# Performance work log

Hardware: AMD Instinct MI355X
Metric: run time of the kernel (lower is better)

The kernel has to match this reference:

```python
import jax, jax.numpy as jnp
import numpy as np

ALPHA = 1.0
EPS = 1e-12  # tf.nn.l2_normalize epsilon
N, IN_DIM, UNITS = 8192, 1, 64


def setup_inputs() -> dict:
    key = jax.random.key(0)
    k1, k2 = jax.random.split(key)
    inputs = jax.random.normal(k1, (N, IN_DIM), dtype=jnp.float32)
    W = jax.random.normal(k2, (IN_DIM, UNITS), dtype=jnp.float32) * (1.0 / np.sqrt(IN_DIM))
    b = jnp.zeros((UNITS,), dtype=jnp.float32)
    return {"inputs": inputs, "W": W, "b": b}


def reference(inputs, W, b):
    # Dense projection (activation='linear')
    emb = inputs @ W + b  # [N, D]
    # Pairwise cosine similarity, computed as normalized matmul instead of
    # materializing the original [N, N, D] broadcast tensors.
    norm = jnp.sqrt(jnp.maximum(jnp.sum(emb * emb, axis=-1, keepdims=True), EPS))
    xn = emb / norm  # [N, D]
    cos = xn @ xn.T  # [N, N] cosine similarity
    # tf pairwise_sim = -cos; loss = 1 - |pairwise_sim| = 1 - |cos|
    loss = 1.0 - jnp.abs(cos)
    loss = jnp.max(loss, axis=-1)  # [N]
    loss = jnp.mean(loss)
    aux_loss = ALPHA * (-loss)  # layer returns -loss, scaled by alpha via add_loss
    return emb, aux_loss
```

## Files before the change

kernel.cpp:

```cpp
#include <hip/hip_runtime.h>
#include <math.h>
#include <float.h>

#define NROWS 8192
#define D     64
#define EPSN  1e-12f
#define TI    8
#define NBLK  (NROWS / TI)
#define JPT   (NROWS / 256)

__device__ __forceinline__ float wave_reduce_sum(float v) {
    #pragma unroll
    for (int m = 1; m < 64; m <<= 1) v += __shfl_xor(v, m, 64);
    return v;
}

__global__ __launch_bounds__(256) void k_main(
        const float* __restrict__ x, const float* __restrict__ W,
        const float* __restrict__ b, float* __restrict__ emb,
        float* __restrict__ partial) {
    __shared__ float red[TI][257];
    __shared__ float red2[TI][17];
    __shared__ float l8[TI];
    const int tid = threadIdx.x;
    const int blk = blockIdx.x;
    const int i0  = blk * TI;
    const int ln  = tid & 63;

    if (tid < TI * 16) {
        const int r  = tid >> 4;
        const int c4 = tid & 15;
        const float xr = x[i0 + r];
        const float4 w4 = ((const float4*)W)[c4];
        const float4 b4 = ((const float4*)b)[c4];
        float4 e;
        e.x = fmaf(xr, w4.x, b4.x);
        e.y = fmaf(xr, w4.y, b4.y);
        e.z = fmaf(xr, w4.z, b4.z);
        e.w = fmaf(xr, w4.w, b4.w);
        ((float4*)emb)[i0 * 16 + tid] = e;
    }

    const float wv = W[ln], bv = b[ln];
    const float wTw = wave_reduce_sum(wv * wv);
    const float wTb = wave_reduce_sum(wv * bv);
    const float bTb = wave_reduce_sum(bv * bv);

    const float xi_l = x[i0 + (ln & 7)];
    const float Af  = fmaf(xi_l, wTw, wTb);
    const float Cf  = fmaf(xi_l, wTb, bTb);
    const float cf  = Cf / Af;
    const float aAf = fabsf(Af);

    float p[JPT], q[JPT];
    #pragma unroll
    for (int k4 = 0; k4 < JPT / 4; ++k4) {
        const float4 v4 = ((const float4*)x)[tid + k4 * 256];
        const float vs[4] = {v4.x, v4.y, v4.z, v4.w};
        #pragma unroll
        for (int e = 0; e < 4; ++e) {
            const float v   = vs[e];
            const float nsq = fmaf(v, fmaf(v, wTw, 2.0f * wTb), bTb);
            const float iv  = rsqrtf(fmaxf(nsq, EPSN));
            q[k4 * 4 + e] = iv;
            p[k4 * 4 + e] = v * iv;
        }
    }

    #pragma unroll
    for (int ii = 0; ii < TI; ++ii) {
        const float absA = __shfl(aAf, ii, 64);
        const float c    = __shfl(cf,  ii, 64);
        const float C    = __shfl(Cf,  ii, 64);
        float mm;
        if (absA > 1e-12f) {
            float m0 = FLT_MAX, m1 = FLT_MAX, m2 = FLT_MAX, m3 = FLT_MAX;
            #pragma unroll
            for (int k = 0; k < JPT; k += 8) {
                const float t0 = fmaf(c, q[k    ], p[k    ]);
                const float t1 = fmaf(c, q[k + 1], p[k + 1]);
                const float t2 = fmaf(c, q[k + 2], p[k + 2]);
                const float t3 = fmaf(c, q[k + 3], p[k + 3]);
                const float t4 = fmaf(c, q[k + 4], p[k + 4]);
                const float t5 = fmaf(c, q[k + 5], p[k + 5]);
                const float t6 = fmaf(c, q[k + 6], p[k + 6]);
                const float t7 = fmaf(c, q[k + 7], p[k + 7]);
                m0 = fminf(m0, fminf(fabsf(t0), fabsf(t1)));
                m1 = fminf(m1, fminf(fabsf(t2), fabsf(t3)));
                m2 = fminf(m2, fminf(fabsf(t4), fabsf(t5)));
                m3 = fminf(m3, fminf(fabsf(t6), fabsf(t7)));
            }
            mm = absA * fminf(fminf(m0, m1), fminf(m2, m3));
        } else {
            float m0 = FLT_MAX, m1 = FLT_MAX;
            #pragma unroll
            for (int k = 0; k < JPT; k += 2) {
                m0 = fminf(m0, q[k]);
                m1 = fminf(m1, q[k + 1]);
            }
            mm = fabsf(C) * fminf(m0, m1);
        }
        red[ii][tid] = mm;
    }
    __syncthreads();

    if (tid < TI * 16) {
        const int ii = tid >> 4, s = tid & 15;
        float mn = red[ii][s];
        #pragma unroll
        for (int t = 1; t < 16; ++t) mn = fminf(mn, red[ii][t * 16 + s]);
        red2[ii][s] = mn;
    }
    __syncthreads();

    if (tid < TI) {
        float mn = red2[tid][0];
        #pragma unroll
        for (int t = 1; t < 16; ++t) mn = fminf(mn, red2[tid][t]);
        const float xi  = x[i0 + tid];
        const float nsq = fmaf(xi, fmaf(xi, wTw, 2.0f * wTb), bTb);
        l8[tid] = 1.0f - mn * rsqrtf(fmaxf(nsq, EPSN));
    }
    __syncthreads();
    if (tid == 0) {
        float s = 0.0f;
        #pragma unroll
        for (int t = 0; t < TI; ++t) s += l8[t];
        partial[blk] = s;
    }
}

__global__ void k_fin(const float* __restrict__ partial, float* __restrict__ aux) {
    __shared__ float s4[4];
    const int tid = threadIdx.x;
    float v = (partial[tid] + partial[tid + 256]) +
              (partial[tid + 512] + partial[tid + 768]);
    v = wave_reduce_sum(v);
    if ((tid & 63) == 0) s4[tid >> 6] = v;
    __syncthreads();
    if (tid == 0) aux[0] = -((s4[0] + s4[1] + s4[2] + s4[3]) / (float)NROWS);
}

extern "C" void kernel_launch(void* const* d_in, const int* in_sizes, int n_in,
                              void* d_out, int out_size, void* d_ws, size_t ws_size,
                              hipStream_t stream) {
    const float* x = (const float*)d_in[0];
    const float* W = (const float*)d_in[1];
    const float* b = (const float*)d_in[2];

    float* emb = (float*)d_out;
    float* aux = (float*)d_out + NROWS * D;

    float* partial = (float*)d_ws;

    k_main<<<NBLK, 256, 0, stream>>>(x, W, b, emb, partial);
    k_fin<<<1, 256, 0, stream>>>(partial, aux);
}
```

Measured before the change: 13.25 us.

## Double rows per loss block and move embedding write into final-reduce kernel

Raises rows per block from 8 to 16, which halves the loss grid to 512 blocks so each block's per-thread normalization of all 8192 x values is amortized over twice as many rows. The embedding store is taken out of the loss kernel and merged with the final reduction into a second kernel of 513 blocks, where block 0 sums the 512 partials and the rest write emb. The x loads are hoisted into a register array ahead of the W/b reductions. In exchange, the loss grid of 512 blocks may leave fewer blocks per CU, and the emb store now runs in the second launch after the loss kernel instead of alongside it.

```diff
diff --git a/kernel.cpp b/kernel.cpp
--- a/kernel.cpp
+++ b/kernel.cpp
@@ -5,7 +5,7 @@
 #define NROWS 8192
 #define D     64
 #define EPSN  1e-12f
-#define TI    8
+#define TI    16
 #define NBLK  (NROWS / TI)
 #define JPT   (NROWS / 256)
 
@@ -15,30 +15,25 @@
     return v;
 }
 
-__global__ __launch_bounds__(256) void k_main(
+__global__ __launch_bounds__(256) void k_loss(
         const float* __restrict__ x, const float* __restrict__ W,
-        const float* __restrict__ b, float* __restrict__ emb,
-        float* __restrict__ partial) {
+        const float* __restrict__ b, float* __restrict__ partial) {
     __shared__ float red[TI][257];
     __shared__ float red2[TI][17];
-    __shared__ float l8[TI];
+    __shared__ float l16[TI];
     const int tid = threadIdx.x;
     const int blk = blockIdx.x;
     const int i0  = blk * TI;
     const int ln  = tid & 63;
 
-    if (tid < TI * 16) {
-        const int r  = tid >> 4;
-        const int c4 = tid & 15;
-        const float xr = x[i0 + r];
-        const float4 w4 = ((const float4*)W)[c4];
-        const float4 b4 = ((const float4*)b)[c4];
-        float4 e;
-        e.x = fmaf(xr, w4.x, b4.x);
-        e.y = fmaf(xr, w4.y, b4.y);
-        e.z = fmaf(xr, w4.z, b4.z);
-        e.w = fmaf(xr, w4.w, b4.w);
-        ((float4*)emb)[i0 * 16 + tid] = e;
+    float xv[JPT];
+    #pragma unroll
+    for (int k4 = 0; k4 < JPT / 4; ++k4) {
+        const float4 v4 = ((const float4*)x)[tid + k4 * 256];
+        xv[k4 * 4 + 0] = v4.x;
+        xv[k4 * 4 + 1] = v4.y;
+        xv[k4 * 4 + 2] = v4.z;
+        xv[k4 * 4 + 3] = v4.w;
     }
 
     const float wv = W[ln], bv = b[ln];
@@ -46,7 +41,7 @@
     const float wTb = wave_reduce_sum(wv * bv);
     const float bTb = wave_reduce_sum(bv * bv);
 
-    const float xi_l = x[i0 + (ln & 7)];
+    const float xi_l = x[i0 + (ln & 15)];
     const float Af  = fmaf(xi_l, wTw, wTb);
     const float Cf  = fmaf(xi_l, wTb, bTb);
     const float cf  = Cf / Af;
@@ -54,17 +49,12 @@
 
     float p[JPT], q[JPT];
     #pragma unroll
-    for (int k4 = 0; k4 < JPT / 4; ++k4) {
-        const float4 v4 = ((const float4*)x)[tid + k4 * 256];
-        const float vs[4] = {v4.x, v4.y, v4.z, v4.w};
-        #pragma unroll
-        for (int e = 0; e < 4; ++e) {
-            const float v   = vs[e];
-            const float nsq = fmaf(v, fmaf(v, wTw, 2.0f * wTb), bTb);
-            const float iv  = rsqrtf(fmaxf(nsq, EPSN));
-            q[k4 * 4 + e] = iv;
-            p[k4 * 4 + e] = v * iv;
-        }
+    for (int k = 0; k < JPT; ++k) {
+        const float v   = xv[k];
+        const float nsq = fmaf(v, fmaf(v, wTw, 2.0f * wTb), bTb);
+        const float iv  = rsqrtf(fmaxf(nsq, EPSN));
+        q[k] = iv;
+        p[k] = v * iv;
     }
 
     #pragma unroll
@@ -104,7 +94,7 @@
     }
     __syncthreads();
 
-    if (tid < TI * 16) {
+    {
         const int ii = tid >> 4, s = tid & 15;
         float mn = red[ii][s];
         #pragma unroll
@@ -119,26 +109,49 @@
         for (int t = 1; t < 16; ++t) mn = fminf(mn, red2[tid][t]);
         const float xi  = x[i0 + tid];
         const float nsq = fmaf(xi, fmaf(xi, wTw, 2.0f * wTb), bTb);
-        l8[tid] = 1.0f - mn * rsqrtf(fmaxf(nsq, EPSN));
+        l16[tid] = 1.0f - mn * rsqrtf(fmaxf(nsq, EPSN));
     }
     __syncthreads();
     if (tid == 0) {
         float s = 0.0f;
         #pragma unroll
-        for (int t = 0; t < TI; ++t) s += l8[t];
+        for (int t = 0; t < TI; ++t) s += l16[t];
         partial[blk] = s;
     }
 }
 
-__global__ void k_fin(const float* __restrict__ partial, float* __restrict__ aux) {
-    __shared__ float s4[4];
+__global__ __launch_bounds__(256) void k_emb_fin(
+        const float* __restrict__ x, const float* __restrict__ W,
+        const float* __restrict__ b, const float* __restrict__ partial,
+        float* __restrict__ emb, float* __restrict__ aux) {
     const int tid = threadIdx.x;
-    float v = (partial[tid] + partial[tid + 256]) +
-              (partial[tid + 512] + partial[tid + 768]);
-    v = wave_reduce_sum(v);
-    if ((tid & 63) == 0) s4[tid >> 6] = v;
-    __syncthreads();
-    if (tid == 0) aux[0] = -((s4[0] + s4[1] + s4[2] + s4[3]) / (float)NROWS);
+    const int blk = blockIdx.x;
+
+    if (blk == 0) {
+        if (tid < 64) {
+            const float4 a = ((const float4*)partial)[tid * 2];
+            const float4 c = ((const float4*)partial)[tid * 2 + 1];
+            const float s = ((a.x + a.y) + (a.z + a.w)) +
+                            ((c.x + c.y) + (c.z + c.w));
+            const float tot = wave_reduce_sum(s);
+            if (tid == 0) aux[0] = -(tot / (float)NROWS);
+        }
+        return;
+    }
+
+    const int t  = blk - 1;
+    const int i0 = t * TI;
+    const int r  = tid >> 4;
+    const int c4 = tid & 15;
+    const float xr = x[i0 + r];
+    const float4 w4 = ((const float4*)W)[c4];
+    const float4 b4 = ((const float4*)b)[c4];
+    float4 e;
+    e.x = fmaf(xr, w4.x, b4.x);
+    e.y = fmaf(xr, w4.y, b4.y);
+    e.z = fmaf(xr, w4.z, b4.z);
+    e.w = fmaf(xr, w4.w, b4.w);
+    ((float4*)emb)[t * 256 + tid] = e;
 }
 
 extern "C" void kernel_launch(void* const* d_in, const int* in_sizes, int n_in,
@@ -153,6 +166,6 @@
 
     float* partial = (float*)d_ws;
 
-    k_main<<<NBLK, 256, 0, stream>>>(x, W, b, emb, partial);
-    k_fin<<<1, 256, 0, stream>>>(partial, aux);
+    k_loss<<<NBLK, 256, 0, stream>>>(x, W, b, partial);
+    k_emb_fin<<<NBLK + 1, 256, 0, stream>>>(x, W, b, partial, emb, aux);
 }
```

Measured after the change: 13.10 us. No clear change (-1.1%).
